# Kernel tuning notes

Measured on AMD Instinct MI355X. Metric: run time of the kernel, lower is better.

## Reference

```python
import jax, jax.numpy as jnp
import numpy as np

DIM, NH, WS, SR, CTS = 256, 8, 8, 4, 2
HD = DIM // NH
SCALE = HD ** -0.5

def _linear(x, w, b=None):
    y = x @ w.T
    return y + b if b is not None else y

def _ln(x, g, b, eps=1e-5):
    m = jnp.mean(x, -1, keepdims=True)
    v = jnp.mean((x - m) ** 2, -1, keepdims=True)
    return (x - m) / jnp.sqrt(v + eps) * g + b

def _mlp(x, w1, b1, w2, b2):
    return _linear(jax.nn.gelu(_linear(x, w1, b1), approximate=False), w2, b2)

def _pos_emb_rank3(seq_len, w1, b1, w2):
    # PosEmbMLPSwinv1D with rank=3: coords on cube_root(seq) grid, normalized
    s = int(round(seq_len ** (1.0 / 3.0)))
    c = (jnp.arange(s, dtype=jnp.float32) - s // 2) / (s // 2)
    grid = jnp.stack(jnp.meshgrid(c, c, c, indexing='ij'))      # (3,s,s,s)
    tbl = grid.reshape(3, -1).T                                 # (s^3,3)
    return _linear(jax.nn.relu(_linear(tbl, w1, b1)), w2)[None]  # (1,s^3,dim)

def _rel_bias_3d(ws, w1, b1, w2, n_global):
    # PosEmbMLPSwinv3D: CPB-MLP bias over 3D relative coords, 16*sigmoid, zero-pad for carrier tokens
    r = jnp.arange(-(ws - 1), ws, dtype=jnp.float32)
    tbl = jnp.stack(jnp.meshgrid(r, r, r, indexing='ij'), axis=-1) / (ws - 1)
    tbl = tbl * 8.0
    tbl = jnp.sign(tbl) * jnp.log2(jnp.abs(tbl) + 1.0) / np.log2(8.0)
    table = _linear(jax.nn.relu(_linear(tbl.reshape(-1, 3), w1, b1)), w2)  # ((2ws-1)^3, NH)
    coords = jnp.stack(jnp.meshgrid(jnp.arange(ws), jnp.arange(ws), jnp.arange(ws), indexing='ij'))
    cf = coords.reshape(3, -1)
    rel = (cf[:, :, None] - cf[:, None, :]).transpose(1, 2, 0) + (ws - 1)  # (P,P,3)
    idx = rel[..., 0] * (2 * ws - 1) ** 2 + rel[..., 1] * (2 * ws - 1) + rel[..., 2]
    P = ws ** 3
    bias = table[idx.reshape(-1)].reshape(P, P, NH).transpose(2, 0, 1)
    bias = 16.0 * jax.nn.sigmoid(bias)
    return jnp.pad(bias, ((0, 0), (n_global, 0), (n_global, 0)))[None]  # (1,NH,P+g,P+g)

def _win_attn(x, qkv_w, qkv_b, proj_w, proj_b, bias):
    B, N, C = x.shape
    qkv = _linear(x, qkv_w, qkv_b).reshape(B, N, 3, NH, HD).transpose(2, 0, 3, 1, 4)
    q, k, v = qkv[0], qkv[1], qkv[2]
    attn = jax.nn.softmax(jnp.einsum('bhnd,bhmd->bhnm', q, k) * SCALE + bias, axis=-1)
    out = jnp.einsum('bhnm,bhmd->bhnd', attn, v).transpose(0, 2, 1, 3).reshape(B, N, C)
    return _linear(out, proj_w, proj_b)

def _ct_dewindow(ct, W, H, D, ws):
    bs, _, N = ct.shape
    c = ct.reshape(bs, W // ws, H // ws, D // ws, ws, ws, ws, N)
    c = c.transpose(0, 7, 1, 3, 5, 2, 4, 6).reshape(bs, N, W * H * D)
    return c.transpose(0, 2, 1)

def _ct_window(ct, W, H, D, ws):
    bs, _, N = ct.shape
    c = ct.reshape(bs, H // ws, ws, W // ws, ws, D // ws, ws, N)
    return c.transpose(0, 1, 3, 5, 2, 4, 6, 7)

def setup_inputs() -> dict:
    key = jax.random.key(0)
    ks = jax.random.split(key, 48)
    B0 = 1
    nw = SR ** 3
    def w(k, *s):
        return jax.random.normal(k, s, jnp.float32) * 0.02
    def b(k, *s):
        return jax.random.normal(k, s, jnp.float32) * 0.01
    d4 = 4 * DIM
    return {
        'x': jax.random.normal(ks[0], (B0 * nw, WS ** 3, DIM), jnp.float32),
        'ct': jax.random.normal(ks[1], (B0, (CTS * SR) ** 3, DIM), jnp.float32),
        'pe_w1': w(ks[2], 512, 3), 'pe_b1': b(ks[3], 512), 'pe_w2': w(ks[4], DIM, 512),
        'hpe_w1': w(ks[5], 512, 3), 'hpe_b1': b(ks[6], 512), 'hpe_w2': w(ks[7], DIM, 512),
        'hat_n1_g': jnp.ones((DIM,), jnp.float32), 'hat_n1_b': jnp.zeros((DIM,), jnp.float32),
        'hat_qkv_w': w(ks[8], 3 * DIM, DIM), 'hat_qkv_b': b(ks[9], 3 * DIM),
        'hat_proj_w': w(ks[10], DIM, DIM), 'hat_proj_b': b(ks[11], DIM),
        'hat_cpb_w1': w(ks[12], 512, 3), 'hat_cpb_b1': b(ks[13], 512), 'hat_cpb_w2': w(ks[14], NH, 512),
        'hat_n2_g': jnp.ones((DIM,), jnp.float32), 'hat_n2_b': jnp.zeros((DIM,), jnp.float32),
        'hat_fc1_w': w(ks[15], d4, DIM), 'hat_fc1_b': b(ks[16], d4),
        'hat_fc2_w': w(ks[17], DIM, d4), 'hat_fc2_b': b(ks[18], DIM),
        'n1_g': jnp.ones((DIM,), jnp.float32), 'n1_b': jnp.zeros((DIM,), jnp.float32),
        'qkv_w': w(ks[19], 3 * DIM, DIM), 'qkv_b': b(ks[20], 3 * DIM),
        'proj_w': w(ks[21], DIM, DIM), 'proj_b': b(ks[22], DIM),
        'cpb_w1': w(ks[23], 512, 3), 'cpb_b1': b(ks[24], 512), 'cpb_w2': w(ks[25], NH, 512),
        'n2_g': jnp.ones((DIM,), jnp.float32), 'n2_b': jnp.zeros((DIM,), jnp.float32),
        'fc1_w': w(ks[26], d4, DIM), 'fc1_b': b(ks[27], d4),
        'fc2_w': w(ks[28], DIM, d4), 'fc2_b': b(ks[29], DIM),
    }

def reference(x, ct, pe_w1, pe_b1, pe_w2, hpe_w1, hpe_b1, hpe_w2,
              hat_n1_g, hat_n1_b, hat_qkv_w, hat_qkv_b, hat_proj_w, hat_proj_b,
              hat_cpb_w1, hat_cpb_b1, hat_cpb_w2, hat_n2_g, hat_n2_b,
              hat_fc1_w, hat_fc1_b, hat_fc2_w, hat_fc2_b,
              n1_g, n1_b, qkv_w, qkv_b, proj_w, proj_b,
              cpb_w1, cpb_b1, cpb_w2, n2_g, n2_b, fc1_w, fc1_b, fc2_w, fc2_b):
    Bg, Ng, Hg = ct.shape
    G = CTS * SR  # carrier-token global cube side
    x = x + _pos_emb_rank3(x.shape[1], pe_w1, pe_b1, pe_w2)
    # carrier-token global attention (hierarchical path)
    ct = _ct_dewindow(ct, G, G, G, CTS)
    ct = ct + _pos_emb_rank3(ct.shape[1], hpe_w1, hpe_b1, hpe_w2)
    hat_bias = _rel_bias_3d(G, hat_cpb_w1, hat_cpb_b1, hat_cpb_w2, 0)
    ct = ct + _win_attn(_ln(ct, hat_n1_g, hat_n1_b), hat_qkv_w, hat_qkv_b, hat_proj_w, hat_proj_b, hat_bias)
    ct = ct + _mlp(_ln(ct, hat_n2_g, hat_n2_b), hat_fc1_w, hat_fc1_b, hat_fc2_w, hat_fc2_b)
    ct_w = _ct_window(ct, G, G, G, CTS).reshape(x.shape[0], -1, Hg)
    # windowed attention over [carrier tokens ; window tokens]
    x = jnp.concatenate([ct_w, x], axis=1)
    bias = _rel_bias_3d(WS, cpb_w1, cpb_b1, cpb_w2, CTS ** 3)
    x = x + _win_attn(_ln(x, n1_g, n1_b), qkv_w, qkv_b, proj_w, proj_b, bias)
    x = x + _mlp(_ln(x, n2_g, n2_b), fc1_w, fc1_b, fc2_w, fc2_b)
    split = x.shape[1] - WS ** 3
    ctr, x = x[:, :split], x[:, split:]
    return x, ctr.reshape(Bg, Ng, Hg)
```

## Files before the change

### kernel.cpp

```cpp
#include <hip/hip_runtime.h>
#include <hip/hip_bf16.h>
#include <math.h>

typedef __hip_bfloat16 bf16;

#define SCALE_QK 0.17677669529663687f

__device__ __forceinline__ float b2f(bf16 v){ return __bfloat162float(v); }
__device__ __forceinline__ bf16  f2b(float v){ return __float2bfloat16(v); }
__device__ __forceinline__ short bfs(float x){ bf16 b = f2b(x); short s; __builtin_memcpy(&s, &b, 2); return s; }

struct __align__(16) bf16x8 { bf16 v[8]; };

typedef __attribute__((ext_vector_type(8))) short sh8;
typedef __attribute__((ext_vector_type(4))) short sh4;
typedef __attribute__((ext_vector_type(4))) float f4;

#if defined(__has_builtin)
#if __has_builtin(__builtin_amdgcn_mfma_f32_16x16x16bf16_1k)
#define HAS_MFMA16 1
#else
#define HAS_MFMA16 0
#endif
#else
#define HAS_MFMA16 0
#endif

__global__ __launch_bounds__(256) void wcvt10_k(const float* s0, const float* s1, const float* s2, const float* s3,
                                                const float* s4, const float* s5, const float* s6, const float* s7,
                                                const float* s8, const float* s9,
                                                bf16* d0, bf16* d1, bf16* d2, bf16* d3, bf16* d4,
                                                bf16* d5, bf16* d6, bf16* d7, bf16* d8, bf16* d9) {
    const int sizes[10] = {196608, 65536, 262144, 262144, 196608, 65536, 262144, 262144, 131072, 131072};
    int which = blockIdx.y;
    const float* s; bf16* d;
    switch (which) {
        case 0: s = s0; d = d0; break;  case 1: s = s1; d = d1; break;
        case 2: s = s2; d = d2; break;  case 3: s = s3; d = d3; break;
        case 4: s = s4; d = d4; break;  case 5: s = s5; d = d5; break;
        case 6: s = s6; d = d6; break;  case 7: s = s7; d = d7; break;
        case 8: s = s8; d = d8; break;  default: s = s9; d = d9; break;
    }
    int i = blockIdx.x * 256 + threadIdx.x;
    if (i < sizes[which]) d[i] = f2b(s[i]);
}

__global__ __launch_bounds__(256) void hidbuild_k(const float* __restrict__ w1a, const float* __restrict__ b1a,
                                                  const float* __restrict__ w1b, const float* __restrict__ b1b,
                                                  bf16* __restrict__ hidA, bf16* __restrict__ hidB) {
    const float* w1 = blockIdx.y ? w1b : w1a;
    const float* b1 = blockIdx.y ? b1b : b1a;
    bf16* hid       = blockIdx.y ? hidB : hidA;
    int t = blockIdx.x, tid = threadIdx.x;
    int i = t >> 6, j = (t >> 3) & 7, k = t & 7;
    float c0 = (i - 4) * 0.25f, c1 = (j - 4) * 0.25f, c2 = (k - 4) * 0.25f;
    #pragma unroll
    for (int rep = 0; rep < 2; rep++) {
        int jj = tid + rep * 256;
        float h = c0 * w1[jj*3+0] + c1 * w1[jj*3+1] + c2 * w1[jj*3+2] + b1[jj];
        hid[(size_t)t * 512 + jj] = f2b(fmaxf(h, 0.f));
    }
}

__device__ __forceinline__ float cpb_coord(int idx) {
    float v = (idx - 7) * (8.0f / 7.0f);
    return copysignf(log2f(fabsf(v) + 1.0f) * (1.0f / 3.0f), v);
}
__global__ __launch_bounds__(512) void cpbtab_k(const float* __restrict__ w1a, const float* __restrict__ b1a,
                                                const float* __restrict__ w2a, float* __restrict__ taba,
                                                const float* __restrict__ w1b, const float* __restrict__ b1b,
                                                const float* __restrict__ w2b, float* __restrict__ tabb) {
    const float* w1 = blockIdx.y ? w1b : w1a;
    const float* b1 = blockIdx.y ? b1b : b1a;
    const float* w2 = blockIdx.y ? w2b : w2a;
    float* tab      = blockIdx.y ? tabb : taba;
    int t = blockIdx.x, tid = threadIdx.x;
    __shared__ float hid[512];
    int i = t / 225, r = t - i * 225, j = r / 15, k = r - j * 15;
    float x0 = cpb_coord(i), x1 = cpb_coord(j), x2 = cpb_coord(k);
    float h = x0 * w1[tid*3+0] + x1 * w1[tid*3+1] + x2 * w1[tid*3+2] + b1[tid];
    hid[tid] = fmaxf(h, 0.f);
    __syncthreads();
    int h8 = tid >> 6, lane = tid & 63;
    float p = 0.f;
    for (int jj = lane; jj < 512; jj += 64) p += hid[jj] * w2[h8*512 + jj];
    for (int off = 32; off; off >>= 1) p += __shfl_down(p, off);
    if (lane == 0) tab[t * 8 + h8] = p;
}

__global__ __launch_bounds__(256) void biasbuild_k(const float* __restrict__ taba, float* __restrict__ biasQa,
                                                   const float* __restrict__ tabb, float* __restrict__ biasQb) {
    const float* tab = blockIdx.y ? tabb : taba;
    float* biasQ     = blockIdx.y ? biasQb : biasQa;
    int idx = blockIdx.x * 256 + threadIdx.x;
    int h = idx >> 18, rem = idx & 262143;
    int q = rem >> 9, k = rem & 511;
    int qx = q >> 6, qy = (q >> 3) & 7, qz = q & 7;
    int kx = k >> 6, ky = (k >> 3) & 7, kz = k & 7;
    int tidx = ((qx - kx + 7) * 15 + (qy - ky + 7)) * 15 + (qz - kz + 7);
    float v = tab[tidx * 8 + h];
    biasQ[idx] = 16.f / (1.f + __expf(-v));
}

__global__ __launch_bounds__(256) void ct0build_k(const float* __restrict__ ct_in,
                                                  const float* __restrict__ hpe,
                                                  float* __restrict__ ct0) {
    int u = blockIdx.x, c = threadIdx.x;
    int a = u >> 7, cc = (u >> 5) & 3, e = (u >> 4) & 1, b = (u >> 2) & 3, d = (u >> 1) & 1, f = u & 1;
    int t = a * 128 + b * 32 + cc * 8 + d * 4 + e * 2 + f;
    ct0[(size_t)u * 256 + c] = ct_in[(size_t)t * 256 + c] + hpe[(size_t)u * 256 + c];
}

__global__ __launch_bounds__(256) void ln_k(const float* __restrict__ in,
                                            const float* __restrict__ g,
                                            const float* __restrict__ b,
                                            bf16* __restrict__ out) {
    int row = blockIdx.x, c = threadIdx.x;
    float x = in[(size_t)row * 256 + c];
    float s = x, s2 = x * x;
    for (int off = 32; off; off >>= 1) { s += __shfl_down(s, off); s2 += __shfl_down(s2, off); }
    __shared__ float red[8];
    int wid = c >> 6, lane = c & 63;
    if (lane == 0) { red[wid] = s; red[wid + 4] = s2; }
    __syncthreads();
    if (c == 0) { red[0] = red[0] + red[1] + red[2] + red[3]; red[4] = red[4] + red[5] + red[6] + red[7]; }
    __syncthreads();
    float mean = red[0] * (1.f / 256.f);
    float var  = fmaxf(red[4] * (1.f / 256.f) - mean * mean, 0.f);
    float rstd = rsqrtf(var + 1e-5f);
    out[(size_t)row * 256 + c] = f2b((x - mean) * rstd * g[c] + b[c]);
}

template <int MODE>
__global__ __launch_bounds__(256) void gemm_k(const bf16* __restrict__ A,
                                              const bf16* __restrict__ W,
                                              const float* __restrict__ bias,
                                              int M, int N, int K,
                                              float* __restrict__ res,
                                              bf16* __restrict__ outb) {
    __shared__ short As[128 * 40];
    __shared__ short Ws[128 * 40];
    int m0 = blockIdx.y * 128, n0 = blockIdx.x * 128;
    int tid = threadIdx.x;
    int lane = tid & 63, wave = tid >> 6;
    int quad = lane >> 4, m16 = lane & 15;
    int wm = (wave & 1) * 64, wn = (wave >> 1) * 64;
    int arow = tid >> 2, acol = (tid & 3) * 8;

    f4 acc[4][4];
    #pragma unroll
    for (int i = 0; i < 4; i++)
        #pragma unroll
        for (int j = 0; j < 4; j++) acc[i][j] = (f4){0.f, 0.f, 0.f, 0.f};

    for (int k0 = 0; k0 < K; k0 += 32) {
        sh8 a0 = *reinterpret_cast<const sh8*>(A + (size_t)(m0 + arow) * K + k0 + acol);
        sh8 a1 = *reinterpret_cast<const sh8*>(A + (size_t)(m0 + arow + 64) * K + k0 + acol);
        sh8 w0 = *reinterpret_cast<const sh8*>(W + (size_t)(n0 + arow) * K + k0 + acol);
        sh8 w1 = *reinterpret_cast<const sh8*>(W + (size_t)(n0 + arow + 64) * K + k0 + acol);
        __syncthreads();
        *reinterpret_cast<sh8*>(&As[arow * 40 + acol])        = a0;
        *reinterpret_cast<sh8*>(&As[(arow + 64) * 40 + acol]) = a1;
        *reinterpret_cast<sh8*>(&Ws[arow * 40 + acol])        = w0;
        *reinterpret_cast<sh8*>(&Ws[(arow + 64) * 40 + acol]) = w1;
        __syncthreads();
        sh8 af[4], bf[4];
        #pragma unroll
        for (int mi = 0; mi < 4; mi++)
            af[mi] = *reinterpret_cast<const sh8*>(&As[(wm + mi * 16 + m16) * 40 + quad * 8]);
        #pragma unroll
        for (int ni = 0; ni < 4; ni++)
            bf[ni] = *reinterpret_cast<const sh8*>(&Ws[(wn + ni * 16 + m16) * 40 + quad * 8]);
        #pragma unroll
        for (int mi = 0; mi < 4; mi++)
            #pragma unroll
            for (int ni = 0; ni < 4; ni++)
                acc[mi][ni] = __builtin_amdgcn_mfma_f32_16x16x32_bf16(af[mi], bf[ni], acc[mi][ni], 0, 0, 0);
    }
    (void)M;

    #pragma unroll
    for (int mi = 0; mi < 4; mi++) {
        #pragma unroll
        for (int r = 0; r < 4; r++) {
            int gm = m0 + wm + mi * 16 + quad * 4 + r;
            #pragma unroll
            for (int ni = 0; ni < 4; ni++) {
                int gn = n0 + wn + ni * 16 + m16;
                float v = acc[mi][ni][r];
                if constexpr (MODE != 3) v += bias[gn];
                if constexpr (MODE == 2)      res[(size_t)gm * N + gn] += v;
                else if constexpr (MODE == 3) res[(size_t)gm * N + gn] = v;
                else if constexpr (MODE == 1) outb[(size_t)gm * N + gn] = f2b(0.5f * v * (1.0f + erff(v * 0.70710678118654752f)));
                else                          outb[(size_t)gm * N + gn] = f2b(v);
            }
        }
    }
}

#define VSTR 548
#define FIXM 24.0f
__global__ __launch_bounds__(512) void flash_k(const bf16* __restrict__ qkv,
                                               const float* __restrict__ biasQ,
                                               bf16* __restrict__ out,
                                               int N, int glob) {
    int wh = blockIdx.x, w = wh >> 3, h = wh & 7;
    int qs = blockIdx.y, QS = gridDim.y;
    int tid = threadIdx.x;
    int lane = tid & 63, wave = tid >> 6;
    int quad = lane >> 4, qcol = lane & 15;
    const int NT32 = (N + 31) & ~31;

    __shared__ bf16  Vt[32 * VSTR];
    __shared__ float Osm[8 * 528];
#if !HAS_MFMA16
    __shared__ float Ps[8][16 * 17];
#endif

    for (int i = tid; i < NT32 * 4; i += 512) {
        int tok = i >> 2, seg = i & 3;
        if (tok < N) {
            const bf16* vp = qkv + ((size_t)(w * N + tok)) * 768 + 512 + h * 32 + seg * 8;
            bf16x8 vv = *reinterpret_cast<const bf16x8*>(vp);
            #pragma unroll
            for (int e = 0; e < 8; e++) Vt[(seg * 8 + e) * VSTR + tok] = vv.v[e];
        } else {
            bf16 z = f2b(0.f);
            #pragma unroll
            for (int e = 0; e < 8; e++) Vt[(seg * 8 + e) * VSTR + tok] = z;
        }
    }
    __syncthreads();

    const bf16* qbase = qkv + ((size_t)w * N) * 768 + h * 32;
    const bf16* kbase = qbase + 256;
    int nqt = (N + 15) >> 4, nkt = NT32 >> 5;
    int npt = (nqt + 1) >> 1;

    for (int pp = wave + 8 * qs; pp < npt; pp += 8 * QS) {
        int qA = pp * 32 + qcol;
        int qB = qA + 16;
        int qrA = (qA < N) ? qA : (N - 1);
        int qrB = (qB < N) ? qB : (N - 1);
        sh8 qfA = *reinterpret_cast<const sh8*>(qbase + (size_t)qrA * 768 + quad * 8);
        sh8 qfB = *reinterpret_cast<const sh8*>(qbase + (size_t)qrB * 768 + quad * 8);
        f4 O0A = {0.f,0.f,0.f,0.f}, O1A = {0.f,0.f,0.f,0.f};
        f4 O0B = {0.f,0.f,0.f,0.f}, O1B = {0.f,0.f,0.f,0.f};
        float lA = 0.f, lB = 0.f;
        bool vA = (qA >= glob) && (qA < N);
        bool vB = (qB >= glob) && (qB < N);
        const float* browA = biasQ + (((size_t)h << 9) + (size_t)(vA ? (qA - glob) : 0)) * 512 - glob;
        const float* browB = biasQ + (((size_t)h << 9) + (size_t)(vB ? (qB - glob) : 0)) * 512 - glob;

        sh8 kf0, kf1;
        {
            int k0 = qcol, k1 = 16 + qcol;
            kf0 = *reinterpret_cast<const sh8*>(kbase + (size_t)((k0 < N) ? k0 : (N - 1)) * 768 + quad * 8);
            kf1 = *reinterpret_cast<const sh8*>(kbase + (size_t)((k1 < N) ? k1 : (N - 1)) * 768 + quad * 8);
        }

        for (int kt = 0; kt < nkt; kt++) {
            int bt = kt * 32;
            sh8 c0 = kf0, c1 = kf1;
            if (kt + 1 < nkt) {
                int n0 = bt + 32 + qcol, n1 = bt + 48 + qcol;
                kf0 = *reinterpret_cast<const sh8*>(kbase + (size_t)((n0 < N) ? n0 : (N - 1)) * 768 + quad * 8);
                kf1 = *reinterpret_cast<const sh8*>(kbase + (size_t)((n1 < N) ? n1 : (N - 1)) * 768 + quad * 8);
            }
            f4 z = {0.f, 0.f, 0.f, 0.f};
            f4 s0A = __builtin_amdgcn_mfma_f32_16x16x32_bf16(c0, qfA, z, 0, 0, 0);
            f4 s1A = __builtin_amdgcn_mfma_f32_16x16x32_bf16(c1, qfA, z, 0, 0, 0);
            f4 s0B = __builtin_amdgcn_mfma_f32_16x16x32_bf16(c0, qfB, z, 0, 0, 0);
            f4 s1B = __builtin_amdgcn_mfma_f32_16x16x32_bf16(c1, qfB, z, 0, 0, 0);

            int tg0 = bt + quad * 4, tg1 = bt + 16 + quad * 4;
            bool val0 = tg0 < N, val1 = tg1 < N;
            f4 bb0A = z, bb1A = z, bb0B = z, bb1B = z;
            if (vA && tg0 >= glob)               bb0A = *reinterpret_cast<const f4*>(browA + tg0);
            if (vA && tg1 >= glob && tg1 < N)    bb1A = *reinterpret_cast<const f4*>(browA + tg1);
            if (vB && tg0 >= glob)               bb0B = *reinterpret_cast<const f4*>(browB + tg0);
            if (vB && tg1 >= glob && tg1 < N)    bb1B = *reinterpret_cast<const f4*>(browB + tg1);

            float pA0[4], pA1[4], pB0[4], pB1[4];
            #pragma unroll
            for (int r = 0; r < 4; r++) {
                pA0[r] = val0 ? __expf(fmaf(s0A[r], SCALE_QK, bb0A[r]) - FIXM) : 0.f;
                pA1[r] = val1 ? __expf(fmaf(s1A[r], SCALE_QK, bb1A[r]) - FIXM) : 0.f;
                pB0[r] = val0 ? __expf(fmaf(s0B[r], SCALE_QK, bb0B[r]) - FIXM) : 0.f;
                pB1[r] = val1 ? __expf(fmaf(s1B[r], SCALE_QK, bb1B[r]) - FIXM) : 0.f;
            }
            #pragma unroll
            for (int r = 0; r < 4; r++) { lA += pA0[r] + pA1[r]; lB += pB0[r] + pB1[r]; }

#if HAS_MFMA16
            sh4 pf0A, pf1A, pf0B, pf1B;
            #pragma unroll
            for (int r = 0; r < 4; r++) {
                pf0A[r] = bfs(pA0[r]); pf1A[r] = bfs(pA1[r]);
                pf0B[r] = bfs(pB0[r]); pf1B[r] = bfs(pB1[r]);
            }
            sh4 v00 = *reinterpret_cast<const sh4*>(&Vt[qcol * VSTR + bt + quad * 4]);
            sh4 v10 = *reinterpret_cast<const sh4*>(&Vt[qcol * VSTR + bt + 16 + quad * 4]);
            sh4 v01 = *reinterpret_cast<const sh4*>(&Vt[(qcol + 16) * VSTR + bt + quad * 4]);
            sh4 v11 = *reinterpret_cast<const sh4*>(&Vt[(qcol + 16) * VSTR + bt + 16 + quad * 4]);
            O0A = __builtin_amdgcn_mfma_f32_16x16x16bf16_1k(v00, pf0A, O0A, 0, 0, 0);
            O0A = __builtin_amdgcn_mfma_f32_16x16x16bf16_1k(v10, pf1A, O0A, 0, 0, 0);
            O1A = __builtin_amdgcn_mfma_f32_16x16x16bf16_1k(v01, pf0A, O1A, 0, 0, 0);
            O1A = __builtin_amdgcn_mfma_f32_16x16x16bf16_1k(v11, pf1A, O1A, 0, 0, 0);
            O0B = __builtin_amdgcn_mfma_f32_16x16x16bf16_1k(v00, pf0B, O0B, 0, 0, 0);
            O0B = __builtin_amdgcn_mfma_f32_16x16x16bf16_1k(v10, pf1B, O0B, 0, 0, 0);
            O1B = __builtin_amdgcn_mfma_f32_16x16x16bf16_1k(v01, pf0B, O1B, 0, 0, 0);
            O1B = __builtin_amdgcn_mfma_f32_16x16x16bf16_1k(v11, pf1B, O1B, 0, 0, 0);
#else
            {
                const float* phA[2] = {pA0, pA1};
                const float* phB[2] = {pB0, pB1};
                for (int t = 0; t < 2; t++) {
                    const float* const* ph = t ? phB : phA;
                    for (int half = 0; half < 2; half++) {
                        #pragma unroll
                        for (int r = 0; r < 4; r++) Ps[wave][(quad * 4 + r) * 17 + qcol] = ph[half][r];
                        __builtin_amdgcn_wave_barrier();
                        sh8 pbig, va, vb;
                        #pragma unroll
                        for (int j = 0; j < 8; j++) {
                            int tl = quad * 8 + j;
                            float pv = (quad < 2) ? Ps[wave][tl * 17 + qcol] : 0.f;
                            pbig[j] = bfs(pv);
                            bf16 a0 = (quad < 2) ? Vt[qcol * VSTR + bt + half * 16 + tl] : f2b(0.f);
                            bf16 a1 = (quad < 2) ? Vt[(qcol + 16) * VSTR + bt + half * 16 + tl] : f2b(0.f);
                            short t0, t1;
                            __builtin_memcpy(&t0, &a0, 2); __builtin_memcpy(&t1, &a1, 2);
                            va[j] = t0; vb[j] = t1;
                        }
                        if (t == 0) {
                            O0A = __builtin_amdgcn_mfma_f32_16x16x32_bf16(va, pbig, O0A, 0, 0, 0);
                            O1A = __builtin_amdgcn_mfma_f32_16x16x32_bf16(vb, pbig, O1A, 0, 0, 0);
                        } else {
                            O0B = __builtin_amdgcn_mfma_f32_16x16x32_bf16(va, pbig, O0B, 0, 0, 0);
                            O1B = __builtin_amdgcn_mfma_f32_16x16x32_bf16(vb, pbig, O1B, 0, 0, 0);
                        }
                        __builtin_amdgcn_wave_barrier();
                    }
                }
            }
#endif
        }

        lA += __shfl_xor(lA, 16); lA += __shfl_xor(lA, 32);
        lB += __shfl_xor(lB, 16); lB += __shfl_xor(lB, 32);
        float rlA = 1.f / lA, rlB = 1.f / lB;
        int row = lane >> 2, dseg = (lane & 3) * 8;

        #pragma unroll
        for (int r = 0; r < 4; r++) {
            Osm[wave * 528 + qcol * 33 + quad * 4 + r]      = O0A[r] * rlA;
            Osm[wave * 528 + qcol * 33 + 16 + quad * 4 + r] = O1A[r] * rlA;
        }
        __builtin_amdgcn_wave_barrier();
        {
            int q_out = pp * 32 + row;
            if (q_out < N) {
                bf16x8 ov;
                #pragma unroll
                for (int e = 0; e < 8; e++) ov.v[e] = f2b(Osm[wave * 528 + row * 33 + dseg + e]);
                *reinterpret_cast<bf16x8*>(out + ((size_t)(w * N + q_out)) * 256 + h * 32 + dseg) = ov;
            }
        }
        __builtin_amdgcn_wave_barrier();

        #pragma unroll
        for (int r = 0; r < 4; r++) {
            Osm[wave * 528 + qcol * 33 + quad * 4 + r]      = O0B[r] * rlB;
            Osm[wave * 528 + qcol * 33 + 16 + quad * 4 + r] = O1B[r] * rlB;
        }
        __builtin_amdgcn_wave_barrier();
        {
            int q_out = pp * 32 + 16 + row;
            if (q_out < N) {
                bf16x8 ov;
                #pragma unroll
                for (int e = 0; e < 8; e++) ov.v[e] = f2b(Osm[wave * 528 + row * 33 + dseg + e]);
                *reinterpret_cast<bf16x8*>(out + ((size_t)(w * N + q_out)) * 256 + h * 32 + dseg) = ov;
            }
        }
        __builtin_amdgcn_wave_barrier();
    }
}

__global__ __launch_bounds__(256) void xcatbuild_k(const float* __restrict__ x_in,
                                                   const float* __restrict__ pe,
                                                   const float* __restrict__ ct2,
                                                   float* __restrict__ xcat) {
    int row = blockIdx.x, w = row / 520, p = row - w * 520, c = threadIdx.x;
    float v;
    if (p < 8) {
        int P = w >> 4, Q = (w >> 2) & 3, R = w & 3;
        int S = p >> 2, T = (p >> 1) & 1, U = p & 1;
        int t = P * 128 + S * 64 + Q * 16 + T * 8 + R * 2 + U;
        v = ct2[(size_t)t * 256 + c];
    } else {
        int t = p - 8;
        v = x_in[((size_t)w * 512 + t) * 256 + c] + pe[(size_t)t * 256 + c];
    }
    xcat[(size_t)row * 256 + c] = v;
}

__global__ __launch_bounds__(256) void outbuild_k(const float* __restrict__ xcat,
                                                  float* __restrict__ out) {
    int row = blockIdx.x, w = row / 520, p = row - w * 520, c = threadIdx.x;
    float v = xcat[(size_t)row * 256 + c];
    if (p >= 8) out[((size_t)(w * 512) + (p - 8)) * 256 + c] = v;
    else        out[(size_t)8388608 + ((size_t)(w * 8) + p) * 256 + c] = v;
}

extern "C" void kernel_launch(void* const* d_in, const int* in_sizes, int n_in,
                              void* d_out, int out_size, void* d_ws, size_t ws_size,
                              hipStream_t stream) {
    const float* x          = (const float*)d_in[0];
    const float* ct         = (const float*)d_in[1];
    const float* pe_w1      = (const float*)d_in[2];
    const float* pe_b1      = (const float*)d_in[3];
    const float* pe_w2      = (const float*)d_in[4];
    const float* hpe_w1     = (const float*)d_in[5];
    const float* hpe_b1     = (const float*)d_in[6];
    const float* hpe_w2     = (const float*)d_in[7];
    const float* hat_n1_g   = (const float*)d_in[8];
    const float* hat_n1_b   = (const float*)d_in[9];
    const float* hat_qkv_w  = (const float*)d_in[10];
    const float* hat_qkv_b  = (const float*)d_in[11];
    const float* hat_proj_w = (const float*)d_in[12];
    const float* hat_proj_b = (const float*)d_in[13];
    const float* hat_cpb_w1 = (const float*)d_in[14];
    const float* hat_cpb_b1 = (const float*)d_in[15];
    const float* hat_cpb_w2 = (const float*)d_in[16];
    const float* hat_n2_g   = (const float*)d_in[17];
    const float* hat_n2_b   = (const float*)d_in[18];
    const float* hat_fc1_w  = (const float*)d_in[19];
    const float* hat_fc1_b  = (const float*)d_in[20];
    const float* hat_fc2_w  = (const float*)d_in[21];
    const float* hat_fc2_b  = (const float*)d_in[22];
    const float* n1_g       = (const float*)d_in[23];
    const float* n1_b       = (const float*)d_in[24];
    const float* qkv_w      = (const float*)d_in[25];
    const float* qkv_b      = (const float*)d_in[26];
    const float* proj_w     = (const float*)d_in[27];
    const float* proj_b     = (const float*)d_in[28];
    const float* cpb_w1     = (const float*)d_in[29];
    const float* cpb_b1     = (const float*)d_in[30];
    const float* cpb_w2     = (const float*)d_in[31];
    const float* n2_g       = (const float*)d_in[32];
    const float* n2_b       = (const float*)d_in[33];
    const float* fc1_w      = (const float*)d_in[34];
    const float* fc1_b      = (const float*)d_in[35];
    const float* fc2_w      = (const float*)d_in[36];
    const float* fc2_b      = (const float*)d_in[37];
    (void)in_sizes; (void)n_in; (void)out_size;

    char* base = (char*)d_ws;
    size_t off = 0;
    auto alloc = [&](size_t bytes) -> void* {
        void* p = base + off;
        off += (bytes + 255) & ~(size_t)255;
        return p;
    };
    float* pe        = (float*)alloc(512 * 256 * 4);
    float* hpe       = (float*)alloc(512 * 256 * 4);
    float* tab_hat   = (float*)alloc(3375 * 8 * 4);
    float* tab2      = (float*)alloc(3375 * 8 * 4);
    float* biasQ2    = (float*)alloc((size_t)8 * 512 * 512 * 4);
    float* ct0       = (float*)alloc(512 * 256 * 4);
    bf16* wb_hqkv  = (bf16*)alloc(768 * 256 * 2);
    bf16* wb_hproj = (bf16*)alloc(256 * 256 * 2);
    bf16* wb_hfc1  = (bf16*)alloc(1024 * 256 * 2);
    bf16* wb_hfc2  = (bf16*)alloc(256 * 1024 * 2);
    bf16* wb_qkv   = (bf16*)alloc(768 * 256 * 2);
    bf16* wb_proj  = (bf16*)alloc(256 * 256 * 2);
    bf16* wb_fc1   = (bf16*)alloc(1024 * 256 * 2);
    bf16* wb_fc2   = (bf16*)alloc(256 * 1024 * 2);
    bf16* wb_pew2  = (bf16*)alloc(256 * 512 * 2);
    bf16* wb_hpew2 = (bf16*)alloc(256 * 512 * 2);
    size_t zstart = off;
    bf16*  hidA      = (bf16*)alloc(512 * 512 * 2);
    bf16*  hidB      = (bf16*)alloc(512 * 512 * 2);
    off = zstart;
    float* biasQ_hat = (float*)alloc((size_t)8 * 512 * 512 * 4);
    bf16*  hct_ln    = (bf16*)alloc(512 * 256 * 2);
    bf16*  hqkv      = (bf16*)alloc(512 * 768 * 2);
    bf16*  hat_attn  = (bf16*)alloc(512 * 256 * 2);
    bf16*  hat_hid   = (bf16*)alloc(512 * 1024 * 2);
    off = zstart;
    float* xcat      = (float*)alloc((size_t)64 * 520 * 256 * 4);
    const int S     = (ws_size >= (size_t)150 * 1024 * 1024) ? 1 : 4;
    const int rows  = 33280 / S;
    const int wins  = 64 / S;
    bf16*  xln_b     = (bf16*)alloc((size_t)rows * 256 * 2);
    char*  region_qa = (char*)alloc((size_t)rows * 1024 * 2);
    bf16*  qkv_b_    = (bf16*)region_qa;
    bf16*  attn_b    = (bf16*)(region_qa + (size_t)rows * 768 * 2);
    bf16*  hidden    = (bf16*)region_qa;

    wcvt10_k<<<dim3(1024, 10), 256, 0, stream>>>(hat_qkv_w, hat_proj_w, hat_fc1_w, hat_fc2_w,
                                                 qkv_w, proj_w, fc1_w, fc2_w, pe_w2, hpe_w2,
                                                 wb_hqkv, wb_hproj, wb_hfc1, wb_hfc2,
                                                 wb_qkv, wb_proj, wb_fc1, wb_fc2, wb_pew2, wb_hpew2);

    hidbuild_k<<<dim3(512, 2), 256, 0, stream>>>(pe_w1, pe_b1, hpe_w1, hpe_b1, hidA, hidB);
    gemm_k<3><<<dim3(2, 4), 256, 0, stream>>>(hidA, wb_pew2,  nullptr, 512, 256, 512, pe,  nullptr);
    gemm_k<3><<<dim3(2, 4), 256, 0, stream>>>(hidB, wb_hpew2, nullptr, 512, 256, 512, hpe, nullptr);

    cpbtab_k<<<dim3(3375, 2), 512, 0, stream>>>(hat_cpb_w1, hat_cpb_b1, hat_cpb_w2, tab_hat,
                                                cpb_w1, cpb_b1, cpb_w2, tab2);
    biasbuild_k<<<dim3(8192, 2), 256, 0, stream>>>(tab_hat, biasQ_hat, tab2, biasQ2);

    ct0build_k<<<512, 256, 0, stream>>>(ct, hpe, ct0);
    ln_k<<<512, 256, 0, stream>>>(ct0, hat_n1_g, hat_n1_b, hct_ln);
    gemm_k<0><<<dim3(6, 4), 256, 0, stream>>>(hct_ln, wb_hqkv, hat_qkv_b, 512, 768, 256, nullptr, hqkv);
    flash_k<<<dim3(8, 2), 512, 0, stream>>>(hqkv, biasQ_hat, hat_attn, 512, 0);
    gemm_k<2><<<dim3(2, 4), 256, 0, stream>>>(hat_attn, wb_hproj, hat_proj_b, 512, 256, 256, ct0, nullptr);
    ln_k<<<512, 256, 0, stream>>>(ct0, hat_n2_g, hat_n2_b, hct_ln);
    gemm_k<1><<<dim3(8, 4), 256, 0, stream>>>(hct_ln, wb_hfc1, hat_fc1_b, 512, 1024, 256, nullptr, hat_hid);
    gemm_k<2><<<dim3(2, 4), 256, 0, stream>>>(hat_hid, wb_hfc2, hat_fc2_b, 512, 256, 1024, ct0, nullptr);

    xcatbuild_k<<<33280, 256, 0, stream>>>(x, pe, ct0, xcat);

    for (int s = 0; s < S; s++) {
        float* xc = xcat + (size_t)s * rows * 256;
        ln_k<<<rows, 256, 0, stream>>>(xc, n1_g, n1_b, xln_b);
        gemm_k<0><<<dim3(6, rows / 128), 256, 0, stream>>>(xln_b, wb_qkv, qkv_b, rows, 768, 256, nullptr, qkv_b_);
        flash_k<<<dim3(wins * 8, 2), 512, 0, stream>>>(qkv_b_, biasQ2, attn_b, 520, 8);
        gemm_k<2><<<dim3(2, rows / 128), 256, 0, stream>>>(attn_b, wb_proj, proj_b, rows, 256, 256, xc, nullptr);
    }
    for (int s = 0; s < S; s++) {
        float* xc = xcat + (size_t)s * rows * 256;
        ln_k<<<rows, 256, 0, stream>>>(xc, n2_g, n2_b, xln_b);
        gemm_k<1><<<dim3(8, rows / 128), 256, 0, stream>>>(xln_b, wb_fc1, fc1_b, rows, 1024, 256, nullptr, hidden);
        gemm_k<2><<<dim3(2, rows / 128), 256, 0, stream>>>(hidden, wb_fc2, fc2_b, rows, 256, 1024, xc, nullptr);
    }

    outbuild_k<<<33280, 256, 0, stream>>>(xcat, (float*)d_out);
}
```

Before: 621.0 us.

## Fold softmax offset and log2 scaling into bias table, drop LDS output staging

Pre-transforms the relative bias into log2 space with the fixed max offset subtracted, so the flash kernel computes exp2(fma(s, scale*log2e, bias)) with no per-element subtract or validity select. Masked and carrier-token columns receive constant bias values instead of branches. Odd trailing query tiles skip the B-half MFMAs and exponentials, and query tiles are interleaved across blocks differently. The output is written straight from MFMA registers as bf16x4, removing the Osm shared buffer and its wave barriers. The cost is narrower, less coalesced global stores.

```diff
diff --git a/kernel.cpp b/kernel.cpp
--- a/kernel.cpp
+++ b/kernel.cpp
@@ -11,6 +11,7 @@
 __device__ __forceinline__ short bfs(float x){ bf16 b = f2b(x); short s; __builtin_memcpy(&s, &b, 2); return s; }
 
 struct __align__(16) bf16x8 { bf16 v[8]; };
+struct __align__(8)  bf16x4 { bf16 v[4]; };
 
 typedef __attribute__((ext_vector_type(8))) short sh8;
 typedef __attribute__((ext_vector_type(4))) short sh4;
@@ -24,6 +25,16 @@
 #endif
 #else
 #define HAS_MFMA16 0
+#endif
+
+#if defined(__has_builtin)
+#if __has_builtin(__builtin_amdgcn_exp2f)
+#define EXP2(x) __builtin_amdgcn_exp2f(x)
+#else
+#define EXP2(x) exp2f(x)
+#endif
+#else
+#define EXP2(x) exp2f(x)
 #endif
 
 __global__ __launch_bounds__(256) void wcvt10_k(const float* s0, const float* s1, const float* s2, const float* s3,
@@ -99,7 +110,8 @@
     int kx = k >> 6, ky = (k >> 3) & 7, kz = k & 7;
     int tidx = ((qx - kx + 7) * 15 + (qy - ky + 7)) * 15 + (qz - kz + 7);
     float v = tab[tidx * 8 + h];
-    biasQ[idx] = 16.f / (1.f + __expf(-v));
+    float b = 16.f / (1.f + __expf(-v));
+    biasQ[idx] = (b - 24.0f) * 1.4426950408889634f;
 }
 
 __global__ __launch_bounds__(256) void ct0build_k(const float* __restrict__ ct_in,
@@ -199,7 +211,9 @@
 }
 
 #define VSTR 548
-#define FIXM 24.0f
+#define SC2   0.25503575360579045f
+#define CNB  (-34.62468098133512f)
+#define NEGB (-1.0e30f)
 __global__ __launch_bounds__(512) void flash_k(const bf16* __restrict__ qkv,
                                                const float* __restrict__ biasQ,
                                                bf16* __restrict__ out,
@@ -211,8 +225,7 @@
     int quad = lane >> 4, qcol = lane & 15;
     const int NT32 = (N + 31) & ~31;
 
-    __shared__ bf16  Vt[32 * VSTR];
-    __shared__ float Osm[8 * 528];
+    __shared__ bf16 Vt[32 * VSTR];
 #if !HAS_MFMA16
     __shared__ float Ps[8][16 * 17];
 #endif
@@ -235,10 +248,11 @@
     const bf16* qbase = qkv + ((size_t)w * N) * 768 + h * 32;
     const bf16* kbase = qbase + 256;
     int nqt = (N + 15) >> 4, nkt = NT32 >> 5;
-    int npt = (nqt + 1) >> 1;
-
-    for (int pp = wave + 8 * qs; pp < npt; pp += 8 * QS) {
-        int qA = pp * 32 + qcol;
+    int nun = (nqt + 1) >> 1;
+
+    for (int u = wave * QS + qs; u < nun; u += 8 * QS) {
+        bool hasB = (2 * u + 1 < nqt);
+        int qA = u * 32 + qcol;
         int qB = qA + 16;
         int qrA = (qA < N) ? qA : (N - 1);
         int qrB = (qB < N) ? qB : (N - 1);
@@ -270,121 +284,125 @@
             f4 z = {0.f, 0.f, 0.f, 0.f};
             f4 s0A = __builtin_amdgcn_mfma_f32_16x16x32_bf16(c0, qfA, z, 0, 0, 0);
             f4 s1A = __builtin_amdgcn_mfma_f32_16x16x32_bf16(c1, qfA, z, 0, 0, 0);
-            f4 s0B = __builtin_amdgcn_mfma_f32_16x16x32_bf16(c0, qfB, z, 0, 0, 0);
-            f4 s1B = __builtin_amdgcn_mfma_f32_16x16x32_bf16(c1, qfB, z, 0, 0, 0);
+            f4 s0B = z, s1B = z;
+            if (hasB) {
+                s0B = __builtin_amdgcn_mfma_f32_16x16x32_bf16(c0, qfB, z, 0, 0, 0);
+                s1B = __builtin_amdgcn_mfma_f32_16x16x32_bf16(c1, qfB, z, 0, 0, 0);
+            }
 
             int tg0 = bt + quad * 4, tg1 = bt + 16 + quad * 4;
             bool val0 = tg0 < N, val1 = tg1 < N;
-            f4 bb0A = z, bb1A = z, bb0B = z, bb1B = z;
-            if (vA && tg0 >= glob)               bb0A = *reinterpret_cast<const f4*>(browA + tg0);
-            if (vA && tg1 >= glob && tg1 < N)    bb1A = *reinterpret_cast<const f4*>(browA + tg1);
-            if (vB && tg0 >= glob)               bb0B = *reinterpret_cast<const f4*>(browB + tg0);
-            if (vB && tg1 >= glob && tg1 < N)    bb1B = *reinterpret_cast<const f4*>(browB + tg1);
-
-            float pA0[4], pA1[4], pB0[4], pB1[4];
+            f4 bb0A, bb1A;
+            if (!val0)                    bb0A = (f4){NEGB, NEGB, NEGB, NEGB};
+            else if (vA && tg0 >= glob)   bb0A = *reinterpret_cast<const f4*>(browA + tg0);
+            else                          bb0A = (f4){CNB, CNB, CNB, CNB};
+            if (!val1)                    bb1A = (f4){NEGB, NEGB, NEGB, NEGB};
+            else if (vA && tg1 >= glob)   bb1A = *reinterpret_cast<const f4*>(browA + tg1);
+            else                          bb1A = (f4){CNB, CNB, CNB, CNB};
+
+            float pA[8];
             #pragma unroll
             for (int r = 0; r < 4; r++) {
-                pA0[r] = val0 ? __expf(fmaf(s0A[r], SCALE_QK, bb0A[r]) - FIXM) : 0.f;
-                pA1[r] = val1 ? __expf(fmaf(s1A[r], SCALE_QK, bb1A[r]) - FIXM) : 0.f;
-                pB0[r] = val0 ? __expf(fmaf(s0B[r], SCALE_QK, bb0B[r]) - FIXM) : 0.f;
-                pB1[r] = val1 ? __expf(fmaf(s1B[r], SCALE_QK, bb1B[r]) - FIXM) : 0.f;
-            }
-            #pragma unroll
-            for (int r = 0; r < 4; r++) { lA += pA0[r] + pA1[r]; lB += pB0[r] + pB1[r]; }
+                pA[r]     = EXP2(fmaf(s0A[r], SC2, bb0A[r]));
+                pA[4 + r] = EXP2(fmaf(s1A[r], SC2, bb1A[r]));
+            }
+            #pragma unroll
+            for (int r = 0; r < 8; r++) lA += pA[r];
+
+            float pB[8];
+            if (hasB) {
+                f4 bb0B, bb1B;
+                if (!val0)                    bb0B = (f4){NEGB, NEGB, NEGB, NEGB};
+                else if (vB && tg0 >= glob)   bb0B = *reinterpret_cast<const f4*>(browB + tg0);
+                else                          bb0B = (f4){CNB, CNB, CNB, CNB};
+                if (!val1)                    bb1B = (f4){NEGB, NEGB, NEGB, NEGB};
+                else if (vB && tg1 >= glob)   bb1B = *reinterpret_cast<const f4*>(browB + tg1);
+                else                          bb1B = (f4){CNB, CNB, CNB, CNB};
+                #pragma unroll
+                for (int r = 0; r < 4; r++) {
+                    pB[r]     = EXP2(fmaf(s0B[r], SC2, bb0B[r]));
+                    pB[4 + r] = EXP2(fmaf(s1B[r], SC2, bb1B[r]));
+                }
+                #pragma unroll
+                for (int r = 0; r < 8; r++) lB += pB[r];
+            }
 
 #if HAS_MFMA16
-            sh4 pf0A, pf1A, pf0B, pf1B;
-            #pragma unroll
-            for (int r = 0; r < 4; r++) {
-                pf0A[r] = bfs(pA0[r]); pf1A[r] = bfs(pA1[r]);
-                pf0B[r] = bfs(pB0[r]); pf1B[r] = bfs(pB1[r]);
-            }
             sh4 v00 = *reinterpret_cast<const sh4*>(&Vt[qcol * VSTR + bt + quad * 4]);
             sh4 v10 = *reinterpret_cast<const sh4*>(&Vt[qcol * VSTR + bt + 16 + quad * 4]);
             sh4 v01 = *reinterpret_cast<const sh4*>(&Vt[(qcol + 16) * VSTR + bt + quad * 4]);
             sh4 v11 = *reinterpret_cast<const sh4*>(&Vt[(qcol + 16) * VSTR + bt + 16 + quad * 4]);
+            sh4 pf0A, pf1A;
+            #pragma unroll
+            for (int r = 0; r < 4; r++) { pf0A[r] = bfs(pA[r]); pf1A[r] = bfs(pA[4 + r]); }
             O0A = __builtin_amdgcn_mfma_f32_16x16x16bf16_1k(v00, pf0A, O0A, 0, 0, 0);
             O0A = __builtin_amdgcn_mfma_f32_16x16x16bf16_1k(v10, pf1A, O0A, 0, 0, 0);
             O1A = __builtin_amdgcn_mfma_f32_16x16x16bf16_1k(v01, pf0A, O1A, 0, 0, 0);
             O1A = __builtin_amdgcn_mfma_f32_16x16x16bf16_1k(v11, pf1A, O1A, 0, 0, 0);
-            O0B = __builtin_amdgcn_mfma_f32_16x16x16bf16_1k(v00, pf0B, O0B, 0, 0, 0);
-            O0B = __builtin_amdgcn_mfma_f32_16x16x16bf16_1k(v10, pf1B, O0B, 0, 0, 0);
-            O1B = __builtin_amdgcn_mfma_f32_16x16x16bf16_1k(v01, pf0B, O1B, 0, 0, 0);
-            O1B = __builtin_amdgcn_mfma_f32_16x16x16bf16_1k(v11, pf1B, O1B, 0, 0, 0);
+            if (hasB) {
+                sh4 pf0B, pf1B;
+                #pragma unroll
+                for (int r = 0; r < 4; r++) { pf0B[r] = bfs(pB[r]); pf1B[r] = bfs(pB[4 + r]); }
+                O0B = __builtin_amdgcn_mfma_f32_16x16x16bf16_1k(v00, pf0B, O0B, 0, 0, 0);
+                O0B = __builtin_amdgcn_mfma_f32_16x16x16bf16_1k(v10, pf1B, O0B, 0, 0, 0);
+                O1B = __builtin_amdgcn_mfma_f32_16x16x16bf16_1k(v01, pf0B, O1B, 0, 0, 0);
+                O1B = __builtin_amdgcn_mfma_f32_16x16x16bf16_1k(v11, pf1B, O1B, 0, 0, 0);
+            }
 #else
-            {
-                const float* phA[2] = {pA0, pA1};
-                const float* phB[2] = {pB0, pB1};
-                for (int t = 0; t < 2; t++) {
-                    const float* const* ph = t ? phB : phA;
-                    for (int half = 0; half < 2; half++) {
-                        #pragma unroll
-                        for (int r = 0; r < 4; r++) Ps[wave][(quad * 4 + r) * 17 + qcol] = ph[half][r];
-                        __builtin_amdgcn_wave_barrier();
-                        sh8 pbig, va, vb;
-                        #pragma unroll
-                        for (int j = 0; j < 8; j++) {
-                            int tl = quad * 8 + j;
-                            float pv = (quad < 2) ? Ps[wave][tl * 17 + qcol] : 0.f;
-                            pbig[j] = bfs(pv);
-                            bf16 a0 = (quad < 2) ? Vt[qcol * VSTR + bt + half * 16 + tl] : f2b(0.f);
-                            bf16 a1 = (quad < 2) ? Vt[(qcol + 16) * VSTR + bt + half * 16 + tl] : f2b(0.f);
-                            short t0, t1;
-                            __builtin_memcpy(&t0, &a0, 2); __builtin_memcpy(&t1, &a1, 2);
-                            va[j] = t0; vb[j] = t1;
-                        }
-                        if (t == 0) {
-                            O0A = __builtin_amdgcn_mfma_f32_16x16x32_bf16(va, pbig, O0A, 0, 0, 0);
-                            O1A = __builtin_amdgcn_mfma_f32_16x16x32_bf16(vb, pbig, O1A, 0, 0, 0);
-                        } else {
-                            O0B = __builtin_amdgcn_mfma_f32_16x16x32_bf16(va, pbig, O0B, 0, 0, 0);
-                            O1B = __builtin_amdgcn_mfma_f32_16x16x32_bf16(vb, pbig, O1B, 0, 0, 0);
-                        }
-                        __builtin_amdgcn_wave_barrier();
+            for (int t = 0; t < 2; t++) {
+                if (t == 1 && !hasB) break;
+                const float* ph = t ? pB : pA;
+                for (int half = 0; half < 2; half++) {
+                    #pragma unroll
+                    for (int r = 0; r < 4; r++) Ps[wave][(quad * 4 + r) * 17 + qcol] = ph[half * 4 + r];
+                    __builtin_amdgcn_wave_barrier();
+                    sh8 pbig, va, vb;
+                    #pragma unroll
+                    for (int j = 0; j < 8; j++) {
+                        int tl = quad * 8 + j;
+                        float pv = (quad < 2) ? Ps[wave][tl * 17 + qcol] : 0.f;
+                        pbig[j] = bfs(pv);
+                        bf16 a0 = (quad < 2) ? Vt[qcol * VSTR + bt + half * 16 + tl] : f2b(0.f);
+                        bf16 a1 = (quad < 2) ? Vt[(qcol + 16) * VSTR + bt + half * 16 + tl] : f2b(0.f);
+                        short t0, t1;
+                        __builtin_memcpy(&t0, &a0, 2); __builtin_memcpy(&t1, &a1, 2);
+                        va[j] = t0; vb[j] = t1;
                     }
+                    if (t == 0) {
+                        O0A = __builtin_amdgcn_mfma_f32_16x16x32_bf16(va, pbig, O0A, 0, 0, 0);
+                        O1A = __builtin_amdgcn_mfma_f32_16x16x32_bf16(vb, pbig, O1A, 0, 0, 0);
+                    } else {
+                        O0B = __builtin_amdgcn_mfma_f32_16x16x32_bf16(va, pbig, O0B, 0, 0, 0);
+                        O1B = __builtin_amdgcn_mfma_f32_16x16x32_bf16(vb, pbig, O1B, 0, 0, 0);
+                    }
+                    __builtin_amdgcn_wave_barrier();
                 }
             }
 #endif
         }
 
         lA += __shfl_xor(lA, 16); lA += __shfl_xor(lA, 32);
-        lB += __shfl_xor(lB, 16); lB += __shfl_xor(lB, 32);
-        float rlA = 1.f / lA, rlB = 1.f / lB;
-        int row = lane >> 2, dseg = (lane & 3) * 8;
-
-        #pragma unroll
-        for (int r = 0; r < 4; r++) {
-            Osm[wave * 528 + qcol * 33 + quad * 4 + r]      = O0A[r] * rlA;
-            Osm[wave * 528 + qcol * 33 + 16 + quad * 4 + r] = O1A[r] * rlA;
+        float rlA = 1.f / lA;
+        if (qA < N) {
+            bf16x4 o0, o1;
+            #pragma unroll
+            for (int r = 0; r < 4; r++) { o0.v[r] = f2b(O0A[r] * rlA); o1.v[r] = f2b(O1A[r] * rlA); }
+            bf16* op = out + ((size_t)(w * N + qA)) * 256 + h * 32 + quad * 4;
+            *reinterpret_cast<bf16x4*>(op)      = o0;
+            *reinterpret_cast<bf16x4*>(op + 16) = o1;
         }
-        __builtin_amdgcn_wave_barrier();
-        {
-            int q_out = pp * 32 + row;
-            if (q_out < N) {
-                bf16x8 ov;
+        if (hasB) {
+            lB += __shfl_xor(lB, 16); lB += __shfl_xor(lB, 32);
+            float rlB = 1.f / lB;
+            if (qB < N) {
+                bf16x4 o0, o1;
                 #pragma unroll
-                for (int e = 0; e < 8; e++) ov.v[e] = f2b(Osm[wave * 528 + row * 33 + dseg + e]);
-                *reinterpret_cast<bf16x8*>(out + ((size_t)(w * N + q_out)) * 256 + h * 32 + dseg) = ov;
+                for (int r = 0; r < 4; r++) { o0.v[r] = f2b(O0B[r] * rlB); o1.v[r] = f2b(O1B[r] * rlB); }
+                bf16* op = out + ((size_t)(w * N + qB)) * 256 + h * 32 + quad * 4;
+                *reinterpret_cast<bf16x4*>(op)      = o0;
+                *reinterpret_cast<bf16x4*>(op + 16) = o1;
             }
         }
-        __builtin_amdgcn_wave_barrier();
-
-        #pragma unroll
-        for (int r = 0; r < 4; r++) {
-            Osm[wave * 528 + qcol * 33 + quad * 4 + r]      = O0B[r] * rlB;
-            Osm[wave * 528 + qcol * 33 + 16 + quad * 4 + r] = O1B[r] * rlB;
-        }
-        __builtin_amdgcn_wave_barrier();
-        {
-            int q_out = pp * 32 + 16 + row;
-            if (q_out < N) {
-                bf16x8 ov;
-                #pragma unroll
-                for (int e = 0; e < 8; e++) ov.v[e] = f2b(Osm[wave * 528 + row * 33 + dseg + e]);
-                *reinterpret_cast<bf16x8*>(out + ((size_t)(w * N + q_out)) * 256 + h * 32 + dseg) = ov;
-            }
-        }
-        __builtin_amdgcn_wave_barrier();
     }
 }
 
```

Measured after the change: 624.1 us. No clear change (+0.5%).
